# Performance work log

Measured on AMD Instinct MI355X. Metric: run time of the kernel, lower is better.

## Reference

```python
import jax, jax.numpy as jnp
import numpy as np
import math

N_LEVELS = 16
F_PER_LEVEL = 2
LOG2_T = 19
T = 1 << LOG2_T
BASE_RES = 16
MAX_RES = 2048
PER_LEVEL_SCALE = (MAX_RES / BASE_RES) ** (1.0 / (N_LEVELS - 1))
BOUND = 0.5
PRIMES = (np.uint32(1), np.uint32(2654435761), np.uint32(805459861))


def _weight_norm(v, g):
    # w = g * v / ||v||_row (torch weight_norm over dim=1)
    return v * (g / jnp.linalg.norm(v, axis=1))[:, None]


def _softplus100(x):
    # torch Softplus(beta=100)
    return jax.nn.softplus(100.0 * x) * 0.01


def hashgrid_encode(x01, table):
    # x01: [N,3] in [0,1]; table: [L, T, F]
    feats = []
    for l in range(N_LEVELS):
        scale = BASE_RES * (PER_LEVEL_SCALE ** l) - 1.0  # tcnn grid scale
        res = int(math.ceil(scale)) + 1
        pos = x01 * scale + 0.5
        pos_floor = jnp.floor(pos)
        w = pos - pos_floor                      # [N,3] trilinear fracs
        c0 = pos_floor.astype(jnp.uint32)        # [N,3] base corner
        dense = (res ** 3) <= T                  # static per level
        acc = jnp.zeros((x01.shape[0], F_PER_LEVEL), dtype=table.dtype)
        for corner in range(8):
            off = [(corner >> d) & 1 for d in range(3)]
            cx = c0[:, 0] + np.uint32(off[0])
            cy = c0[:, 1] + np.uint32(off[1])
            cz = c0[:, 2] + np.uint32(off[2])
            if dense:
                idx = cx + cy * np.uint32(res) + cz * np.uint32(res * res)
            else:
                idx = (cx * PRIMES[0]) ^ (cy * PRIMES[1]) ^ (cz * PRIMES[2])
                idx = idx & np.uint32(T - 1)
            wc = ((w[:, 0] if off[0] else 1.0 - w[:, 0])
                  * (w[:, 1] if off[1] else 1.0 - w[:, 1])
                  * (w[:, 2] if off[2] else 1.0 - w[:, 2]))
            acc = acc + wc[:, None] * table[l, idx.astype(jnp.int32)]
        feats.append(acc)
    return jnp.concatenate(feats, axis=-1)  # [N, 32]


def setup_inputs() -> dict:
    key = jax.random.key(0)
    ks = jax.random.split(key, 4)
    N = 2 ** 21
    x = jax.random.uniform(ks[0], (N, 3), jnp.float32, -BOUND, BOUND)
    table = jax.random.uniform(ks[1], (N_LEVELS, T, F_PER_LEVEL), jnp.float32, -1e-4, 1e-4)
    d_in, d_hid, d_out = 35, 64, 13
    v1 = jax.random.normal(ks[2], (d_hid, d_in), jnp.float32) * (math.sqrt(2) / math.sqrt(d_hid))
    v2 = jax.random.normal(ks[3], (d_out, d_hid), jnp.float32) * 1e-4 + math.sqrt(math.pi) / math.sqrt(d_hid)
    g1 = jnp.linalg.norm(v1, axis=1)
    g2 = jnp.linalg.norm(v2, axis=1)
    b1 = jnp.zeros((d_hid,), jnp.float32)
    b2 = jnp.full((d_out,), -0.5, jnp.float32)  # -sphere_init_radius
    return {"x": x, "table": table, "v1": v1, "g1": g1, "b1": b1,
            "v2": v2, "g2": g2, "b2": b2}


def reference(x, table, v1, g1, b1, v2, g2, b2):
    x01 = jnp.clip((x + BOUND) / (2.0 * BOUND), 0.0, 1.0)
    enc = hashgrid_encode(x01, table)            # [N, 32]
    h = jnp.concatenate([x, enc], axis=1)        # [N, 35]
    w1 = _weight_norm(v1, g1)
    w2 = _weight_norm(v2, g2)
    h = _softplus100(h @ w1.T + b1)
    out = h @ w2.T + b2                          # [N, 13]
    return out
```

## Files before the change

### kernel.cpp

```cpp
#include <hip/hip_runtime.h>
#include <hip/hip_fp16.h>
#include <cstdint>
#include <cmath>

#define NLEV 16
#define NHASH 11
#define NDENSE 5
#define TBL (1u << 19)
#define NBKT 32768

struct LevelParams {
    float scale[NLEV];
    uint32_t res[NLEV];
    uint32_t hashed_mask;
};

__global__ __launch_bounds__(128) void prep_weights(
    const float* __restrict__ v1, const float* __restrict__ g1,
    const float* __restrict__ v2, const float* __restrict__ g2,
    float* __restrict__ w1t, float* __restrict__ w2n)
{
    int t = threadIdx.x;
    if (t < 64) {
        float s = 0.f;
        #pragma unroll
        for (int k = 0; k < 35; ++k) { float v = v1[t*35 + k]; s += v*v; }
        float f = g1[t] / sqrtf(s);
        #pragma unroll
        for (int k = 0; k < 35; ++k) w1t[k*64 + t] = v1[t*35 + k] * f;
    } else if (t < 77) {
        int r = t - 64;
        float s = 0.f;
        #pragma unroll
        for (int k = 0; k < 64; ++k) { float v = v2[r*64 + k]; s += v*v; }
        float f = g2[r] / sqrtf(s);
        #pragma unroll
        for (int k = 0; k < 64; ++k) w2n[r*64 + k] = v2[r*64 + k] * f;
    }
}

__global__ __launch_bounds__(256) void pack_table(
    const float2* __restrict__ in, uint32_t* __restrict__ out, int n)
{
    int i = blockIdx.x * 256 + threadIdx.x;
    if (i < n) {
        float2 v = in[i];
        __half2 h = __floats2half2_rn(v.x, v.y);
        out[i] = *reinterpret_cast<uint32_t*>(&h);
    }
}

__device__ __forceinline__ uint32_t bucket_key(float u0, float u1, float u2)
{
    uint32_t a = min(31u, (uint32_t)(u0 * 32.f));
    uint32_t b = min(31u, (uint32_t)(u1 * 32.f));
    uint32_t c = min(31u, (uint32_t)(u2 * 32.f));
    return (a << 10) | (b << 5) | c;
}

__device__ __forceinline__ void load_u(const float* __restrict__ x, int pp,
                                       float& u0, float& u1, float& u2)
{
    float x0 = x[3*(size_t)pp + 0];
    float x1 = x[3*(size_t)pp + 1];
    float x2 = x[3*(size_t)pp + 2];
    u0 = fminf(fmaxf(x0 + 0.5f, 0.f), 1.f);
    u1 = fminf(fmaxf(x1 + 0.5f, 0.f), 1.f);
    u2 = fminf(fmaxf(x2 + 0.5f, 0.f), 1.f);
}

__global__ __launch_bounds__(256) void hist_kernel(
    const float* __restrict__ x, uint32_t* __restrict__ hist, int N)
{
    int i = blockIdx.x * 256 + threadIdx.x;
    if (i < N) {
        float u0, u1, u2;
        load_u(x, i, u0, u1, u2);
        atomicAdd(&hist[bucket_key(u0, u1, u2)], 1u);
    }
}

__global__ __launch_bounds__(1024) void scan_hist(
    const uint32_t* __restrict__ hist, uint32_t* __restrict__ offs)
{
    __shared__ uint32_t part[1024];
    int t = threadIdx.x;
    uint32_t loc[32];
    uint32_t s = 0;
    #pragma unroll
    for (int k = 0; k < 32; ++k) { loc[k] = s; s += hist[t*32 + k]; }
    part[t] = s;
    __syncthreads();
    for (int d = 1; d < 1024; d <<= 1) {
        uint32_t v = (t >= d) ? part[t - d] : 0u;
        __syncthreads();
        part[t] += v;
        __syncthreads();
    }
    uint32_t base = (t > 0) ? part[t - 1] : 0u;
    #pragma unroll
    for (int k = 0; k < 32; ++k) offs[t*32 + k] = base + loc[k];
}

__global__ __launch_bounds__(256) void scatter_kernel(
    const float* __restrict__ x, uint32_t* __restrict__ offs,
    float4* __restrict__ xs4, int N)
{
    int i = blockIdx.x * 256 + threadIdx.x;
    if (i < N) {
        float x0 = x[3*(size_t)i + 0];
        float x1 = x[3*(size_t)i + 1];
        float x2 = x[3*(size_t)i + 2];
        float u0 = fminf(fmaxf(x0 + 0.5f, 0.f), 1.f);
        float u1 = fminf(fmaxf(x1 + 0.5f, 0.f), 1.f);
        float u2 = fminf(fmaxf(x2 + 0.5f, 0.f), 1.f);
        uint32_t pos = atomicAdd(&offs[bucket_key(u0, u1, u2)], 1u);
        xs4[pos] = make_float4(x0, x1, x2, __int_as_float(i));
    }
}

__device__ __forceinline__ void encode_one(
    float u0, float u1, float u2, float s, uint32_t res, bool hashed,
    const uint32_t* __restrict__ tl, float& a0, float& a1)
{
    float px = u0 * s + 0.5f;
    float py = u1 * s + 0.5f;
    float pz = u2 * s + 0.5f;
    float fx = floorf(px), fy = floorf(py), fz = floorf(pz);
    float wx1 = px - fx, wy1 = py - fy, wz1 = pz - fz;
    float wx0 = 1.f - wx1, wy0 = 1.f - wy1, wz0 = 1.f - wz1;
    uint32_t cx = (uint32_t)fx, cy = (uint32_t)fy, cz = (uint32_t)fz;

    uint32_t ix0, ix1, iy0, iy1, iz0, iz1;
    if (hashed) {
        ix0 = cx;                 ix1 = cx + 1u;
        iy0 = cy * 2654435761u;   iy1 = (cy + 1u) * 2654435761u;
        iz0 = cz * 805459861u;    iz1 = (cz + 1u) * 805459861u;
    } else {
        ix0 = cx;                 ix1 = cx + 1u;
        iy0 = cy * res;           iy1 = iy0 + res;
        uint32_t rr = res * res;
        iz0 = cz * rr;            iz1 = iz0 + rr;
    }

    uint32_t idxs[8];
    #pragma unroll
    for (int c = 0; c < 8; ++c) {
        uint32_t jx = (c & 1) ? ix1 : ix0;
        uint32_t jy = (c & 2) ? iy1 : iy0;
        uint32_t jz = (c & 4) ? iz1 : iz0;
        idxs[c] = hashed ? ((jx ^ jy ^ jz) & (TBL - 1u)) : (jx + jy + jz);
    }
    uint32_t raw[8];
    #pragma unroll
    for (int c = 0; c < 8; ++c) raw[c] = tl[idxs[c]];

    float wxy00 = wx0*wy0, wxy10 = wx1*wy0, wxy01 = wx0*wy1, wxy11 = wx1*wy1;
    a0 = 0.f; a1 = 0.f;
    #pragma unroll
    for (int c = 0; c < 8; ++c) {
        float wxy = (c & 2) ? ((c & 1) ? wxy11 : wxy01)
                            : ((c & 1) ? wxy10 : wxy00);
        float w = wxy * ((c & 4) ? wz1 : wz0);
        __half2 hv = *reinterpret_cast<__half2*>(&raw[c]);
        float2 v = __half22float2(hv);
        a0 += w * v.x;
        a1 += w * v.y;
    }
}

template <int SORTED>
__global__ __launch_bounds__(256) void encode_hashed(
    const float* __restrict__ x, const float4* __restrict__ xs4,
    const uint32_t* __restrict__ tpk,
    uint32_t* __restrict__ feats, int N, int chunks_per_level, LevelParams P)
{
    int bid = blockIdx.x;
    int li = bid / chunks_per_level;
    int l = li + NDENSE;
    int base = (bid - li * chunks_per_level) * 512 + threadIdx.x;
    const uint32_t* tl = tpk + (size_t)l * TBL;
    float s = P.scale[l];

    int p[2] = { base, base + 256 };

    uint2 Q[2][4];
    uint32_t par[2];
    float wx0[2], wx1[2], wyz[2][4];

    #pragma unroll
    for (int t = 0; t < 2; ++t) {
        int pp = (p[t] < N) ? p[t] : (N - 1);
        float u0, u1, u2;
        if (SORTED) {
            float4 v4 = xs4[pp];
            u0 = fminf(fmaxf(v4.x + 0.5f, 0.f), 1.f);
            u1 = fminf(fmaxf(v4.y + 0.5f, 0.f), 1.f);
            u2 = fminf(fmaxf(v4.z + 0.5f, 0.f), 1.f);
        } else {
            load_u(x, pp, u0, u1, u2);
        }

        float px = u0 * s + 0.5f;
        float py = u1 * s + 0.5f;
        float pz = u2 * s + 0.5f;
        float fx = floorf(px), fy = floorf(py), fz = floorf(pz);
        float a1f = px - fx, b1f = py - fy, c1f = pz - fz;
        wx1[t] = a1f; wx0[t] = 1.f - a1f;
        float wy0 = 1.f - b1f, wz0 = 1.f - c1f;
        uint32_t cx = (uint32_t)fx, cy = (uint32_t)fy, cz = (uint32_t)fz;

        wyz[t][0] = wy0 * wz0;
        wyz[t][1] = b1f * wz0;
        wyz[t][2] = wy0 * c1f;
        wyz[t][3] = b1f * c1f;

        uint32_t hy0 = cy * 2654435761u, hy1 = (cy + 1u) * 2654435761u;
        uint32_t hz0 = cz * 805459861u,  hz1 = (cz + 1u) * 805459861u;
        uint32_t r[4] = { hy0 ^ hz0, hy1 ^ hz0, hy0 ^ hz1, hy1 ^ hz1 };

        par[t] = 0u;
        if (!(cx & 1u)) {
            #pragma unroll
            for (int k = 0; k < 4; ++k) {
                uint32_t v0 = (cx ^ r[k]) & (TBL - 1u);
                Q[t][k] = *reinterpret_cast<const uint2*>(tl + (v0 & ~1u));
                par[t] |= (v0 & 1u) << k;
            }
        } else {
            #pragma unroll
            for (int k = 0; k < 4; ++k) {
                uint32_t v0 = (cx ^ r[k]) & (TBL - 1u);
                uint32_t v1 = ((cx + 1u) ^ r[k]) & (TBL - 1u);
                Q[t][k].x = tl[v0];
                Q[t][k].y = tl[v1];
            }
        }
    }

    #pragma unroll
    for (int t = 0; t < 2; ++t) {
        float a0 = 0.f, a1 = 0.f;
        #pragma unroll
        for (int k = 0; k < 4; ++k) {
            uint32_t swap = (par[t] >> k) & 1u;
            uint32_t b0 = swap ? Q[t][k].y : Q[t][k].x;
            uint32_t b1 = swap ? Q[t][k].x : Q[t][k].y;
            __half2 h0 = *reinterpret_cast<__half2*>(&b0);
            __half2 h1 = *reinterpret_cast<__half2*>(&b1);
            float2 c0 = __half22float2(h0);
            float2 c1 = __half22float2(h1);
            a0 += wyz[t][k] * (wx0[t] * c0.x + wx1[t] * c1.x);
            a1 += wyz[t][k] * (wx0[t] * c0.y + wx1[t] * c1.y);
        }
        __half2 hv = __floats2half2_rn(a0, a1);
        if (p[t] < N) {
            __builtin_nontemporal_store(*reinterpret_cast<uint32_t*>(&hv),
                                        &feats[(size_t)li * N + p[t]]);
        }
    }
}

template <int SORTED>
__global__ __launch_bounds__(256) void mlp_dense(
    const float* __restrict__ x, const float4* __restrict__ xs4,
    const uint32_t* __restrict__ tpk,
    const uint32_t* __restrict__ feats,
    const float* __restrict__ w1t,
    const float* __restrict__ b1,
    const float* __restrict__ w2,
    const float* __restrict__ b2,
    float* __restrict__ out, int N, LevelParams P)
{
    int p = blockIdx.x * 256 + threadIdx.x;
    bool valid = (p < N);
    int pp = valid ? p : (N - 1);

    float x0, x1, x2;
    int oidx;
    if (SORTED) {
        float4 v4 = xs4[pp];
        x0 = v4.x; x1 = v4.y; x2 = v4.z;
        oidx = __float_as_int(v4.w);
    } else {
        x0 = x[3*(size_t)pp + 0];
        x1 = x[3*(size_t)pp + 1];
        x2 = x[3*(size_t)pp + 2];
        oidx = pp;
    }
    float u0 = fminf(fmaxf(x0 + 0.5f, 0.f), 1.f);
    float u1 = fminf(fmaxf(x1 + 0.5f, 0.f), 1.f);
    float u2 = fminf(fmaxf(x2 + 0.5f, 0.f), 1.f);

    uint32_t rf[NHASH];
    #pragma unroll
    for (int li = 0; li < NHASH; ++li) rf[li] = feats[(size_t)li * N + pp];

    float h[64];
    #pragma unroll
    for (int j = 0; j < 64; ++j) {
        h[j] = b1[j] + x0 * w1t[0*64 + j] + x1 * w1t[1*64 + j] + x2 * w1t[2*64 + j];
    }

    #pragma unroll
    for (int l = 0; l < NDENSE; ++l) {
        const uint32_t* tl = tpk + (size_t)l * TBL;
        float a0, a1;
        encode_one(u0, u1, u2, P.scale[l], P.res[l], false, tl, a0, a1);
        const float* c0p = w1t + (3 + 2*l) * 64;
        const float* c1p = c0p + 64;
        #pragma unroll
        for (int j = 0; j < 64; ++j) h[j] += a0 * c0p[j] + a1 * c1p[j];
    }

    #pragma unroll
    for (int li = 0; li < NHASH; ++li) {
        __half2 hv = *reinterpret_cast<__half2*>(&rf[li]);
        float2 f = __half22float2(hv);
        int l = li + NDENSE;
        const float* c0p = w1t + (3 + 2*l) * 64;
        const float* c1p = c0p + 64;
        #pragma unroll
        for (int j = 0; j < 64; ++j) h[j] += f.x * c0p[j] + f.y * c1p[j];
    }

    #pragma unroll
    for (int j = 0; j < 64; ++j) {
        float z = 100.f * h[j];
        float t = __expf(-fabsf(z));
        h[j] = (fmaxf(z, 0.f) + __logf(1.f + t)) * 0.01f;
    }

    float* op = out + (size_t)oidx * 13;
    for (int o = 0; o < 13; ++o) {
        float a = b2[o];
        const float* wr = w2 + o * 64;
        #pragma unroll
        for (int k = 0; k < 64; ++k) a = fmaf(h[k], wr[k], a);
        if (valid) op[o] = a;
    }
}

template <int PACKED>
__global__ __launch_bounds__(256) void sdf_fused(
    const float* __restrict__ x, const void* __restrict__ table,
    const float* __restrict__ w1t, const float* __restrict__ b1,
    const float* __restrict__ w2, const float* __restrict__ b2,
    float* __restrict__ out, int N, LevelParams P)
{
    int i = blockIdx.x * 256 + threadIdx.x;
    bool valid = (i < N);
    int ii = valid ? i : (N - 1);

    float u0, u1, u2;
    float x0 = x[3*(size_t)ii + 0];
    float x1 = x[3*(size_t)ii + 1];
    float x2 = x[3*(size_t)ii + 2];
    u0 = fminf(fmaxf(x0 + 0.5f, 0.f), 1.f);
    u1 = fminf(fmaxf(x1 + 0.5f, 0.f), 1.f);
    u2 = fminf(fmaxf(x2 + 0.5f, 0.f), 1.f);

    float h[64];
    #pragma unroll
    for (int j = 0; j < 64; ++j) {
        h[j] = b1[j] + x0 * w1t[0*64 + j] + x1 * w1t[1*64 + j] + x2 * w1t[2*64 + j];
    }

    for (int l = 0; l < NLEV; ++l) {
        bool hashed = (P.hashed_mask >> l) & 1u;
        float a0, a1;
        if (PACKED) {
            const uint32_t* tl = (const uint32_t*)table + (size_t)l * TBL;
            encode_one(u0, u1, u2, P.scale[l], P.res[l], hashed, tl, a0, a1);
        } else {
            const float* tl = (const float*)table + (size_t)l * (size_t)(TBL * 2u);
            float s = P.scale[l]; uint32_t res = P.res[l];
            float px = u0*s + 0.5f, py = u1*s + 0.5f, pz = u2*s + 0.5f;
            float fx = floorf(px), fy = floorf(py), fz = floorf(pz);
            float wx1 = px-fx, wy1 = py-fy, wz1 = pz-fz;
            float wx0 = 1.f-wx1, wy0 = 1.f-wy1, wz0 = 1.f-wz1;
            uint32_t cx = (uint32_t)fx, cy = (uint32_t)fy, cz = (uint32_t)fz;
            a0 = 0.f; a1 = 0.f;
            #pragma unroll
            for (int c = 0; c < 8; ++c) {
                uint32_t jx = cx + (c & 1);
                uint32_t jy = cy + ((c >> 1) & 1);
                uint32_t jz = cz + ((c >> 2) & 1);
                uint32_t idx = hashed
                    ? ((jx ^ (jy * 2654435761u) ^ (jz * 805459861u)) & (TBL - 1u))
                    : (jx + jy * res + jz * res * res);
                float w = ((c & 1) ? wx1 : wx0) * ((c & 2) ? wy1 : wy0)
                        * ((c & 4) ? wz1 : wz0);
                float2 v = *reinterpret_cast<const float2*>(tl + (size_t)idx * 2u);
                a0 += w * v.x; a1 += w * v.y;
            }
        }
        const float* c0p = w1t + (3 + 2*l) * 64;
        const float* c1p = c0p + 64;
        #pragma unroll
        for (int j = 0; j < 64; ++j) h[j] += a0 * c0p[j] + a1 * c1p[j];
    }

    #pragma unroll
    for (int j = 0; j < 64; ++j) {
        float z = 100.f * h[j];
        float t = __expf(-fabsf(z));
        h[j] = (fmaxf(z, 0.f) + __logf(1.f + t)) * 0.01f;
    }

    float* op = out + (size_t)ii * 13;
    for (int o = 0; o < 13; ++o) {
        float a = b2[o];
        const float* wr = w2 + o * 64;
        #pragma unroll
        for (int k = 0; k < 64; ++k) a += h[k] * wr[k];
        if (valid) op[o] = a;
    }
}

extern "C" void kernel_launch(void* const* d_in, const int* in_sizes, int n_in,
                              void* d_out, int out_size, void* d_ws, size_t ws_size,
                              hipStream_t stream)
{
    const float* x     = (const float*)d_in[0];
    const float* table = (const float*)d_in[1];
    const float* v1    = (const float*)d_in[2];
    const float* g1    = (const float*)d_in[3];
    const float* b1    = (const float*)d_in[4];
    const float* v2    = (const float*)d_in[5];
    const float* g2    = (const float*)d_in[6];
    const float* b2    = (const float*)d_in[7];
    float* out = (float*)d_out;
    int N = in_sizes[0] / 3;

    const int n_entries = NLEV * (int)TBL;
    const size_t packed_bytes = (size_t)n_entries * 4u;
    const size_t xs4_bytes    = (size_t)N * 16u;
    const size_t feats_bytes  = (size_t)NHASH * (size_t)N * 4u;
    const size_t hist_bytes   = (size_t)NBKT * 4u;
    const size_t w_bytes = (35*64 + 13*64) * sizeof(float);

    size_t off_packed = 0;
    size_t off_xs4    = off_packed + packed_bytes;
    size_t off_feats  = off_xs4 + xs4_bytes;
    size_t off_hist   = off_feats + feats_bytes;
    size_t off_offs   = off_hist + hist_bytes;
    size_t off_w      = off_offs + hist_bytes;
    size_t sorted_need = off_w + w_bytes;

    bool sorted_ok = (ws_size >= sorted_need);
    bool two_pass  = (ws_size >= packed_bytes + feats_bytes + w_bytes);
    bool packed_ok = (ws_size >= packed_bytes + w_bytes);

    uint32_t* tpk   = (uint32_t*)((char*)d_ws + off_packed);
    float4*   xs4   = (float4*)((char*)d_ws + off_xs4);
    uint32_t* feats;
    uint32_t* hist  = (uint32_t*)((char*)d_ws + off_hist);
    uint32_t* offs  = (uint32_t*)((char*)d_ws + off_offs);
    float* w1t;
    if (sorted_ok) {
        feats = (uint32_t*)((char*)d_ws + off_feats);
        w1t = (float*)((char*)d_ws + off_w);
    } else if (two_pass) {
        feats = (uint32_t*)((char*)d_ws + packed_bytes);
        w1t = (float*)((char*)d_ws + packed_bytes + feats_bytes);
    } else {
        feats = nullptr;
        w1t = (float*)((char*)d_ws + (packed_ok ? packed_bytes : 0));
    }
    float* w2n = w1t + 35 * 64;

    LevelParams P;
    P.hashed_mask = 0u;
    double pls = pow(128.0, 1.0 / 15.0);
    for (int l = 0; l < NLEV; ++l) {
        double sc = 16.0 * pow(pls, (double)l) - 1.0;
        P.scale[l] = (float)sc;
        uint32_t res = (uint32_t)(ceil(sc)) + 1u;
        P.res[l] = res;
        uint64_t r3 = (uint64_t)res * res * res;
        if (r3 > (uint64_t)TBL) P.hashed_mask |= (1u << l);
    }

    prep_weights<<<1, 128, 0, stream>>>(v1, g1, v2, g2, w1t, w2n);

    int chunks = (N + 255) / 256;
    if (sorted_ok) {
        pack_table<<<(n_entries + 255) / 256, 256, 0, stream>>>(
            (const float2*)table, tpk, n_entries);
        hipMemsetAsync(hist, 0, hist_bytes, stream);
        hist_kernel<<<chunks, 256, 0, stream>>>(x, hist, N);
        scan_hist<<<1, 1024, 0, stream>>>(hist, offs);
        scatter_kernel<<<chunks, 256, 0, stream>>>(x, offs, xs4, N);
        int chunks2 = (N + 511) / 512;
        encode_hashed<1><<<chunks2 * NHASH, 256, 0, stream>>>(
            x, xs4, tpk, feats, N, chunks2, P);
        mlp_dense<1><<<chunks, 256, 0, stream>>>(
            x, xs4, tpk, feats, w1t, b1, w2n, b2, out, N, P);
    } else if (two_pass) {
        pack_table<<<(n_entries + 255) / 256, 256, 0, stream>>>(
            (const float2*)table, tpk, n_entries);
        int chunks2 = (N + 511) / 512;
        encode_hashed<0><<<chunks2 * NHASH, 256, 0, stream>>>(
            x, nullptr, tpk, feats, N, chunks2, P);
        mlp_dense<0><<<chunks, 256, 0, stream>>>(
            x, nullptr, tpk, feats, w1t, b1, w2n, b2, out, N, P);
    } else if (packed_ok) {
        pack_table<<<(n_entries + 255) / 256, 256, 0, stream>>>(
            (const float2*)table, tpk, n_entries);
        sdf_fused<1><<<chunks, 256, 0, stream>>>(
            x, (const void*)tpk, w1t, b1, w2n, b2, out, N, P);
    } else {
        sdf_fused<0><<<chunks, 256, 0, stream>>>(
            x, (const void*)table, w1t, b1, w2n, b2, out, N, P);
    }
}
```

Baseline: 865.9 us.

## Run MLP layers on MFMA tensor cores with fp16 prepacked weights

Replaces the per-thread scalar fp32 MLP in the sorted path with a wave-level MFMA kernel. Inputs and features are packed as fp16 into LDS, both layers use mfma_f32_16x16x32_f16, and weights are pre-swizzled and zero-padded into fragment layout by prep_weights. The aim is to remove the large scalar FMA cost of the 35x64 and 64x13 matmuls. In exchange, inputs, hidden activations and weights drop to fp16, which adds rounding error.

```diff
diff --git a/kernel.cpp b/kernel.cpp
--- a/kernel.cpp
+++ b/kernel.cpp
@@ -9,16 +9,27 @@
 #define TBL (1u << 19)
 #define NBKT 32768
 
+typedef _Float16 half8 __attribute__((ext_vector_type(8)));
+typedef float f32x4 __attribute__((ext_vector_type(4)));
+
 struct LevelParams {
     float scale[NLEV];
     uint32_t res[NLEV];
     uint32_t hashed_mask;
 };
 
-__global__ __launch_bounds__(128) void prep_weights(
+__device__ __forceinline__ int krow_map(int kr) {
+    if (kr <= 2) return kr;
+    if (kr >= 4 && kr <= 13) return kr - 1;
+    if (kr >= 16 && kr <= 37) return kr - 3;
+    return -1;
+}
+
+__global__ __launch_bounds__(256) void prep_weights(
     const float* __restrict__ v1, const float* __restrict__ g1,
     const float* __restrict__ v2, const float* __restrict__ g2,
-    float* __restrict__ w1t, float* __restrict__ w2n)
+    float* __restrict__ w1t, float* __restrict__ w2n,
+    __half* __restrict__ w1f, __half* __restrict__ w2f)
 {
     int t = threadIdx.x;
     if (t < 64) {
@@ -36,6 +47,22 @@
         float f = g2[r] / sqrtf(s);
         #pragma unroll
         for (int k = 0; k < 64; ++k) w2n[r*64 + k] = v2[r*64 + k] * f;
+    }
+    __syncthreads();
+    for (int i = t; i < 4096; i += 256) {
+        int j = i & 7, lane = (i >> 3) & 63, nt = (i >> 9) & 3, kc = i >> 11;
+        int kr = kc*32 + ((lane >> 4) << 3) + j;
+        int ncol = nt*16 + (lane & 15);
+        int m = krow_map(kr);
+        float val = (m >= 0) ? w1t[m*64 + ncol] : 0.f;
+        w1f[i] = __float2half(val);
+    }
+    for (int i = t; i < 1024; i += 256) {
+        int j = i & 7, lane = (i >> 3) & 63, kc = i >> 9;
+        int kr = kc*32 + ((lane >> 4) << 3) + j;
+        int col = lane & 15;
+        float val = (col < 13) ? w2n[col*64 + kr] : 0.f;
+        w2f[i] = __float2half(val);
     }
 }
 
@@ -183,7 +210,6 @@
     float s = P.scale[l];
 
     int p[2] = { base, base + 256 };
-
     uint2 Q[2][4];
     uint32_t par[2];
     float wx0[2], wx1[2], wyz[2][4];
@@ -261,33 +287,159 @@
     }
 }
 
-template <int SORTED>
-__global__ __launch_bounds__(256) void mlp_dense(
-    const float* __restrict__ x, const float4* __restrict__ xs4,
+__global__ __launch_bounds__(256) void mlp_mfma(
+    const float4* __restrict__ xs4,
     const uint32_t* __restrict__ tpk,
     const uint32_t* __restrict__ feats,
-    const float* __restrict__ w1t,
+    const __half* __restrict__ w1f,
+    const __half* __restrict__ w2f,
     const float* __restrict__ b1,
-    const float* __restrict__ w2,
     const float* __restrict__ b2,
+    float* __restrict__ out, int N, LevelParams P)
+{
+    __shared__ uint4 ldsA[4][512];
+    __shared__ int   ldsI[4][64];
+    int wid = threadIdx.x >> 6, lane = threadIdx.x & 63;
+    int wpt = blockIdx.x * 256 + wid * 64;
+    int pt = wpt + lane;
+    int pp = (pt < N) ? pt : (N - 1);
+
+    float4 v4 = xs4[pp];
+    float x0 = v4.x, x1 = v4.y, x2 = v4.z;
+    ldsI[wid][lane] = __float_as_int(v4.w);
+    float u0 = fminf(fmaxf(x0 + 0.5f, 0.f), 1.f);
+    float u1 = fminf(fmaxf(x1 + 0.5f, 0.f), 1.f);
+    float u2 = fminf(fmaxf(x2 + 0.5f, 0.f), 1.f);
+
+    uint32_t dw[32];
+    #pragma unroll
+    for (int i = 0; i < 32; ++i) dw[i] = 0u;
+    __half2 h01 = __floats2half2_rn(x0, x1);
+    __half2 h2_ = __floats2half2_rn(x2, 0.f);
+    dw[0] = *reinterpret_cast<uint32_t*>(&h01);
+    dw[1] = *reinterpret_cast<uint32_t*>(&h2_);
+    #pragma unroll
+    for (int l = 0; l < NDENSE; ++l) {
+        const uint32_t* tl = tpk + (size_t)l * TBL;
+        float a0, a1;
+        encode_one(u0, u1, u2, P.scale[l], P.res[l], false, tl, a0, a1);
+        __half2 hv = __floats2half2_rn(a0, a1);
+        dw[2 + l] = *reinterpret_cast<uint32_t*>(&hv);
+    }
+    #pragma unroll
+    for (int li = 0; li < NHASH; ++li)
+        dw[8 + li] = feats[(size_t)li * N + pp];
+
+    #pragma unroll
+    for (int c = 0; c < 8; ++c) {
+        uint4 ch = make_uint4(dw[4*c], dw[4*c+1], dw[4*c+2], dw[4*c+3]);
+        ldsA[wid][c*64 + lane] = ch;
+    }
+
+    const uint4* w1f4 = (const uint4*)w1f;
+    half8 bf[4][2];
+    #pragma unroll
+    for (int nt = 0; nt < 4; ++nt)
+        #pragma unroll
+        for (int kc = 0; kc < 2; ++kc) {
+            uint4 u = w1f4[(kc*4 + nt)*64 + lane];
+            bf[nt][kc] = __builtin_bit_cast(half8, u);
+        }
+
+    f32x4 C[4][4];
+    #pragma unroll
+    for (int nt = 0; nt < 4; ++nt) {
+        float bv = b1[nt*16 + (lane & 15)];
+        #pragma unroll
+        for (int m = 0; m < 4; ++m) C[m][nt] = f32x4{bv, bv, bv, bv};
+    }
+
+    #pragma unroll
+    for (int m = 0; m < 4; ++m) {
+        uint4 ua0 = ldsA[wid][((lane >> 4)      )*64 + m*16 + (lane & 15)];
+        uint4 ua1 = ldsA[wid][((lane >> 4) + 4  )*64 + m*16 + (lane & 15)];
+        half8 a0 = __builtin_bit_cast(half8, ua0);
+        half8 a1 = __builtin_bit_cast(half8, ua1);
+        #pragma unroll
+        for (int nt = 0; nt < 4; ++nt) {
+            C[m][nt] = __builtin_amdgcn_mfma_f32_16x16x32_f16(a0, bf[nt][0], C[m][nt], 0, 0, 0);
+            C[m][nt] = __builtin_amdgcn_mfma_f32_16x16x32_f16(a1, bf[nt][1], C[m][nt], 0, 0, 0);
+        }
+    }
+
+    #pragma unroll
+    for (int m = 0; m < 4; ++m)
+        #pragma unroll
+        for (int nt = 0; nt < 4; ++nt)
+            #pragma unroll
+            for (int r = 0; r < 4; ++r) {
+                float z = 100.f * C[m][nt][r];
+                float t = __expf(-fabsf(z));
+                C[m][nt][r] = (fmaxf(z, 0.f) + __logf(1.f + t)) * 0.01f;
+            }
+
+    uint32_t* hl = (uint32_t*)&ldsA[wid][0];
+    bool evenl = (lane & 1) == 0;
+    #pragma unroll
+    for (int m = 0; m < 4; ++m)
+        #pragma unroll
+        for (int nt = 0; nt < 4; ++nt)
+            #pragma unroll
+            for (int r = 0; r < 4; ++r) {
+                float self = C[m][nt][r];
+                float other = __shfl_xor(self, 1);
+                if (evenl) {
+                    __half2 hp = __floats2half2_rn(self, other);
+                    int prow = m*16 + ((lane >> 4) << 2) + r;
+                    int colp = (nt*16 + (lane & 15)) >> 1;
+                    hl[prow*32 + colp] = *reinterpret_cast<uint32_t*>(&hp);
+                }
+            }
+
+    const uint4* w2f4 = (const uint4*)w2f;
+    half8 b2f[2];
+    #pragma unroll
+    for (int kc = 0; kc < 2; ++kc) {
+        uint4 u = w2f4[kc*64 + lane];
+        b2f[kc] = __builtin_bit_cast(half8, u);
+    }
+    int col = lane & 15;
+    float b2v = (col < 13) ? b2[col] : 0.f;
+
+    #pragma unroll
+    for (int m = 0; m < 4; ++m) {
+        uint4 ua0 = ldsA[wid][(m*16 + col)*8 + 0 + (lane >> 4)];
+        uint4 ua1 = ldsA[wid][(m*16 + col)*8 + 4 + (lane >> 4)];
+        f32x4 c2 = f32x4{b2v, b2v, b2v, b2v};
+        c2 = __builtin_amdgcn_mfma_f32_16x16x32_f16(
+                 __builtin_bit_cast(half8, ua0), b2f[0], c2, 0, 0, 0);
+        c2 = __builtin_amdgcn_mfma_f32_16x16x32_f16(
+                 __builtin_bit_cast(half8, ua1), b2f[1], c2, 0, 0, 0);
+        #pragma unroll
+        for (int r = 0; r < 4; ++r) {
+            int prow = m*16 + ((lane >> 4) << 2) + r;
+            if (col < 13 && wpt + prow < N) {
+                int og = ldsI[wid][prow];
+                out[(size_t)og * 13 + col] = c2[r];
+            }
+        }
+    }
+}
+
+__global__ __launch_bounds__(256) void mlp_dense_scalar(
+    const float* __restrict__ x, const uint32_t* __restrict__ tpk,
+    const uint32_t* __restrict__ feats,
+    const float* __restrict__ w1t, const float* __restrict__ b1,
+    const float* __restrict__ w2, const float* __restrict__ b2,
     float* __restrict__ out, int N, LevelParams P)
 {
     int p = blockIdx.x * 256 + threadIdx.x;
     bool valid = (p < N);
     int pp = valid ? p : (N - 1);
 
-    float x0, x1, x2;
-    int oidx;
-    if (SORTED) {
-        float4 v4 = xs4[pp];
-        x0 = v4.x; x1 = v4.y; x2 = v4.z;
-        oidx = __float_as_int(v4.w);
-    } else {
-        x0 = x[3*(size_t)pp + 0];
-        x1 = x[3*(size_t)pp + 1];
-        x2 = x[3*(size_t)pp + 2];
-        oidx = pp;
-    }
+    float x0 = x[3*(size_t)pp + 0];
+    float x1 = x[3*(size_t)pp + 1];
+    float x2 = x[3*(size_t)pp + 2];
     float u0 = fminf(fmaxf(x0 + 0.5f, 0.f), 1.f);
     float u1 = fminf(fmaxf(x1 + 0.5f, 0.f), 1.f);
     float u2 = fminf(fmaxf(x2 + 0.5f, 0.f), 1.f);
@@ -298,9 +450,8 @@
 
     float h[64];
     #pragma unroll
-    for (int j = 0; j < 64; ++j) {
+    for (int j = 0; j < 64; ++j)
         h[j] = b1[j] + x0 * w1t[0*64 + j] + x1 * w1t[1*64 + j] + x2 * w1t[2*64 + j];
-    }
 
     #pragma unroll
     for (int l = 0; l < NDENSE; ++l) {
@@ -312,7 +463,6 @@
         #pragma unroll
         for (int j = 0; j < 64; ++j) h[j] += a0 * c0p[j] + a1 * c1p[j];
     }
-
     #pragma unroll
     for (int li = 0; li < NHASH; ++li) {
         __half2 hv = *reinterpret_cast<__half2*>(&rf[li]);
@@ -323,15 +473,13 @@
         #pragma unroll
         for (int j = 0; j < 64; ++j) h[j] += f.x * c0p[j] + f.y * c1p[j];
     }
-
     #pragma unroll
     for (int j = 0; j < 64; ++j) {
         float z = 100.f * h[j];
         float t = __expf(-fabsf(z));
         h[j] = (fmaxf(z, 0.f) + __logf(1.f + t)) * 0.01f;
     }
-
-    float* op = out + (size_t)oidx * 13;
+    float* op = out + (size_t)pp * 13;
     for (int o = 0; o < 13; ++o) {
         float a = b2[o];
         const float* wr = w2 + o * 64;
@@ -352,19 +500,17 @@
     bool valid = (i < N);
     int ii = valid ? i : (N - 1);
 
-    float u0, u1, u2;
     float x0 = x[3*(size_t)ii + 0];
     float x1 = x[3*(size_t)ii + 1];
     float x2 = x[3*(size_t)ii + 2];
-    u0 = fminf(fmaxf(x0 + 0.5f, 0.f), 1.f);
-    u1 = fminf(fmaxf(x1 + 0.5f, 0.f), 1.f);
-    u2 = fminf(fmaxf(x2 + 0.5f, 0.f), 1.f);
+    float u0 = fminf(fmaxf(x0 + 0.5f, 0.f), 1.f);
+    float u1 = fminf(fmaxf(x1 + 0.5f, 0.f), 1.f);
+    float u2 = fminf(fmaxf(x2 + 0.5f, 0.f), 1.f);
 
     float h[64];
     #pragma unroll
-    for (int j = 0; j < 64; ++j) {
+    for (int j = 0; j < 64; ++j)
         h[j] = b1[j] + x0 * w1t[0*64 + j] + x1 * w1t[1*64 + j] + x2 * w1t[2*64 + j];
-    }
 
     for (int l = 0; l < NLEV; ++l) {
         bool hashed = (P.hashed_mask >> l) & 1u;
@@ -438,7 +584,8 @@
     const size_t xs4_bytes    = (size_t)N * 16u;
     const size_t feats_bytes  = (size_t)NHASH * (size_t)N * 4u;
     const size_t hist_bytes   = (size_t)NBKT * 4u;
-    const size_t w_bytes = (35*64 + 13*64) * sizeof(float);
+    const size_t w_bytes      = (35*64 + 13*64) * sizeof(float);
+    const size_t wf_bytes     = (4096 + 1024) * sizeof(__half);
 
     size_t off_packed = 0;
     size_t off_xs4    = off_packed + packed_bytes;
@@ -446,17 +593,18 @@
     size_t off_hist   = off_feats + feats_bytes;
     size_t off_offs   = off_hist + hist_bytes;
     size_t off_w      = off_offs + hist_bytes;
-    size_t sorted_need = off_w + w_bytes;
+    size_t off_wf     = off_w + w_bytes;
+    size_t sorted_need = off_wf + wf_bytes;
 
     bool sorted_ok = (ws_size >= sorted_need);
-    bool two_pass  = (ws_size >= packed_bytes + feats_bytes + w_bytes);
-    bool packed_ok = (ws_size >= packed_bytes + w_bytes);
+    bool two_pass  = (ws_size >= packed_bytes + feats_bytes + w_bytes + wf_bytes);
+    bool packed_ok = (ws_size >= packed_bytes + w_bytes + wf_bytes);
 
     uint32_t* tpk   = (uint32_t*)((char*)d_ws + off_packed);
     float4*   xs4   = (float4*)((char*)d_ws + off_xs4);
-    uint32_t* feats;
     uint32_t* hist  = (uint32_t*)((char*)d_ws + off_hist);
     uint32_t* offs  = (uint32_t*)((char*)d_ws + off_offs);
+    uint32_t* feats;
     float* w1t;
     if (sorted_ok) {
         feats = (uint32_t*)((char*)d_ws + off_feats);
@@ -469,6 +617,8 @@
         w1t = (float*)((char*)d_ws + (packed_ok ? packed_bytes : 0));
     }
     float* w2n = w1t + 35 * 64;
+    __half* w1f = (__half*)(w2n + 13 * 64);
+    __half* w2f = w1f + 4096;
 
     LevelParams P;
     P.hashed_mask = 0u;
@@ -482,7 +632,7 @@
         if (r3 > (uint64_t)TBL) P.hashed_mask |= (1u << l);
     }
 
-    prep_weights<<<1, 128, 0, stream>>>(v1, g1, v2, g2, w1t, w2n);
+    prep_weights<<<1, 256, 0, stream>>>(v1, g1, v2, g2, w1t, w2n, w1f, w2f);
 
     int chunks = (N + 255) / 256;
     if (sorted_ok) {
@@ -495,16 +645,16 @@
         int chunks2 = (N + 511) / 512;
         encode_hashed<1><<<chunks2 * NHASH, 256, 0, stream>>>(
             x, xs4, tpk, feats, N, chunks2, P);
-        mlp_dense<1><<<chunks, 256, 0, stream>>>(
-            x, xs4, tpk, feats, w1t, b1, w2n, b2, out, N, P);
+        mlp_mfma<<<chunks, 256, 0, stream>>>(
+            xs4, tpk, feats, w1f, w2f, b1, b2, out, N, P);
     } else if (two_pass) {
         pack_table<<<(n_entries + 255) / 256, 256, 0, stream>>>(
             (const float2*)table, tpk, n_entries);
         int chunks2 = (N + 511) / 512;
         encode_hashed<0><<<chunks2 * NHASH, 256, 0, stream>>>(
             x, nullptr, tpk, feats, N, chunks2, P);
-        mlp_dense<0><<<chunks, 256, 0, stream>>>(
-            x, nullptr, tpk, feats, w1t, b1, w2n, b2, out, N, P);
+        mlp_dense_scalar<<<chunks, 256, 0, stream>>>(
+            x, tpk, feats, w1t, b1, w2n, b2, out, N, P);
     } else if (packed_ok) {
         pack_table<<<(n_entries + 255) / 256, 256, 0, stream>>>(
             (const float2*)table, tpk, n_entries);
```

Measured after the change: 739.0 us. 1.17x faster.
